# Performance work log

Hardware: AMD Instinct MI355X
Metric: run time of the kernel (lower is better)

Reference implementation:

```python
import jax, jax.numpy as jnp
import numpy as np

D_MODEL = 1024
N_HEADS = 16
HEAD = D_MODEL // N_HEADS
B, S = 2, 2048


def setup_inputs() -> dict:
    key = jax.random.key(0)
    ks = jax.random.split(key, 9)
    sc = 1.0 / np.sqrt(D_MODEL)
    return {
        "q": jax.random.normal(ks[0], (B, S, D_MODEL), dtype=jnp.float32),
        "k": jax.random.normal(ks[1], (B, S, D_MODEL), dtype=jnp.float32),
        "v": jax.random.normal(ks[2], (B, S, D_MODEL), dtype=jnp.float32),
        "mask": jnp.zeros((S, S), dtype=jnp.float32),
        "Wq": jax.random.normal(ks[3], (D_MODEL, D_MODEL), dtype=jnp.float32) * sc,
        "bq": jnp.zeros((D_MODEL,), dtype=jnp.float32),
        "Wk": jax.random.normal(ks[4], (D_MODEL, D_MODEL), dtype=jnp.float32) * sc,
        "bk": jnp.zeros((D_MODEL,), dtype=jnp.float32),
        "Wv": jax.random.normal(ks[5], (D_MODEL, D_MODEL), dtype=jnp.float32) * sc,
        "bv": jnpp_zeros() if False else jnp.zeros((D_MODEL,), dtype=jnp.float32),
    }


def reference(q, k, v, mask, Wq, bq, Wk, bk, Wv, bv):
    # Linear projections (torch Linear: x @ W.T + b)
    qp = q @ Wq.T + bq  # (B, S, D)
    kp = k @ Wk.T + bk
    vp = v @ Wv.T + bv
    # split heads -> (B, H, S, Hd)
    def split(x):
        return x.reshape(B, S, N_HEADS, HEAD).transpose(0, 2, 1, 3)
    qh, kh, vh = split(qp), split(kp), split(vp)
    scores = jnp.einsum('bhqd,bhkd->bhqk', qh, kh) / np.sqrt(HEAD)
    scores = scores + mask  # additive mask broadcast over (B, H)
    attn = jax.nn.softmax(scores, axis=-1)
    out = jnp.einsum('bhqk,bhkd->bhqd', attn, vh)
    return out.transpose(0, 2, 1, 3).reshape(B, S, D_MODEL)
```

## Files before the change

kernel.cpp:

```cpp
#include <hip/hip_runtime.h>
#include <cstdint>

#define DM 1024
#define NH 16
#define HDIM 64
#define SEQ 2048
#define NB 2
#define L2E 1.44269504f

typedef unsigned short u16;
typedef unsigned int u32;
typedef __attribute__((ext_vector_type(8))) short bf16x8;
typedef __attribute__((ext_vector_type(8))) unsigned short u16x8;
typedef __attribute__((ext_vector_type(4))) unsigned int u32x4;
typedef __attribute__((ext_vector_type(4))) float f32x4;
typedef __attribute__((ext_vector_type(16))) float f32x16;
typedef __attribute__((ext_vector_type(4))) unsigned short u16x4;

__device__ __forceinline__ u16 f2bf(float f) {
  uint32_t x = __float_as_uint(f);
  x += 0x7fffu + ((x >> 16) & 1u);
  return (u16)(x >> 16);
}

__device__ __forceinline__ u32 pack_bf2t(float lo, float hi) {
  return __builtin_amdgcn_perm(__float_as_uint(hi), __float_as_uint(lo), 0x07060302u);
}

__device__ __forceinline__ void gload_lds16(const void* g, void* lds) {
  __builtin_amdgcn_global_load_lds(
      (const __attribute__((address_space(1))) unsigned int*)(uintptr_t)g,
      (__attribute__((address_space(3))) unsigned int*)(uint32_t)(uintptr_t)lds,
      16, 0, 0);
}


__global__ __launch_bounds__(256) void cvt_kernel(
    const float4* __restrict__ s0, const float4* __restrict__ s1, const float4* __restrict__ s2,
    const float4* __restrict__ s3, const float4* __restrict__ s4, const float4* __restrict__ s5,
    u16x4* __restrict__ d0, u16x4* __restrict__ d1, u16x4* __restrict__ d2,
    u16x4* __restrict__ d3, u16x4* __restrict__ d4, u16x4* __restrict__ d5) {
  int i = blockIdx.x * 256 + threadIdx.x;
  const float4* s;
  u16x4* d;
  int off;
  if (i < 3 * 1048576) {
    int seg = i >> 20;
    off = i & 1048575;
    s = seg == 0 ? s0 : (seg == 1 ? s1 : s2);
    d = seg == 0 ? d0 : (seg == 1 ? d1 : d2);
  } else {
    int j = i - 3 * 1048576;
    int seg = j >> 18;
    off = j & 262143;
    s = seg == 0 ? s3 : (seg == 1 ? s4 : s5);
    d = seg == 0 ? d3 : (seg == 1 ? d4 : d5);
  }
  float4 v = s[off];
  u16x4 o = {f2bf(v.x), f2bf(v.y), f2bf(v.z), f2bf(v.w)};
  d[off] = o;
}

__global__ __launch_bounds__(256) void maskprep_kernel(const float* __restrict__ mask,
                                                       u16* __restrict__ maskP) {
  __shared__ float tile[32][257];
  const int t = threadIdx.x;
  const int q0 = blockIdx.x * 32;
#pragma unroll
  for (int ss = 0; ss < 2; ++ss) {
    const int st = blockIdx.y * 2 + ss;
    const int kv0 = st * 256;
    if (ss) __syncthreads();
#pragma unroll
    for (int p = 0; p < 8; ++p) {
      const int row = p * 4 + (t >> 6);
      const int col = (t & 63) * 4;
      *(float4*)&tile[row][col] = *(const float4*)&mask[(size_t)(q0 + row) * SEQ + kv0 + col];
    }
    __syncthreads();
    const int tgl = t >> 5, ql = t & 31;
    u16 outv[32];
#pragma unroll
    for (int i = 0; i < 32; ++i) {
      const int hl = i >> 4, r = i & 15;
      const int kvl = (r & 3) + 8 * (r >> 2) + 4 * hl;
      outv[i] = f2bf(tile[ql][tgl * 32 + kvl] * L2E);
    }
    u16* dst = maskP + ((size_t)(st * 8 + tgl) * SEQ + (q0 + ql)) * 32;
#pragma unroll
    for (int j = 0; j < 4; ++j) *(u16x8*)(dst + 8 * j) = *(const u16x8*)&outv[8 * j];
  }
}

__global__ __launch_bounds__(256) void proj_kernel(
    const u16* __restrict__ Xq, const u16* __restrict__ Xk, const u16* __restrict__ Xv,
    const u16* __restrict__ Wqp, const u16* __restrict__ Wkp, const u16* __restrict__ Wvp,
    const float* __restrict__ bqp, const float* __restrict__ bkp, const float* __restrict__ bvp,
    u16* __restrict__ Qp, u16* __restrict__ Kp, u16* __restrict__ Vt) {
  __shared__ __align__(16) u16 sA[2][128 * 32];
  __shared__ __align__(16) u16 sB[2][128 * 32];
  const int t = threadIdx.x;
  const int w = t >> 6, lane = t & 63, quad = lane >> 4, l16 = lane & 15;
  const int wr = w >> 1, wc = w & 1;
  const int m0 = blockIdx.y * 128, n0 = blockIdx.x * 128;
  const int mode = blockIdx.z;
  const u16* X = mode == 0 ? Xq : (mode == 1 ? Xk : Xv);
  const u16* W = mode == 0 ? Wqp : (mode == 1 ? Wkp : Wvp);
  const float* bias = mode == 0 ? bqp : (mode == 1 ? bkp : bvp);

  f32x4 acc[4][4] = {};
  const int srow = lane >> 2;
  const int scol = (lane & 3) * 16;

#pragma unroll
  for (int j = 0; j < 2; ++j) {
    const int rbase = (w * 2 + j) * 16;
    gload_lds16((const char*)X + ((size_t)(m0 + rbase + srow) * DM) * 2 + scol,
                (char*)sA[0] + rbase * 64);
    gload_lds16((const char*)W + ((size_t)(n0 + rbase + srow) * DM) * 2 + scol,
                (char*)sB[0] + rbase * 64);
  }

  for (int it = 0; it < 32; ++it) {
    const int p = it & 1;
    __syncthreads();
    if (it < 31) {
      const int k0 = (it + 1) * 32;
#pragma unroll
      for (int j = 0; j < 2; ++j) {
        const int rbase = (w * 2 + j) * 16;
        gload_lds16((const char*)X + ((size_t)(m0 + rbase + srow) * DM + k0) * 2 + scol,
                    (char*)sA[p ^ 1] + rbase * 64);
        gload_lds16((const char*)W + ((size_t)(n0 + rbase + srow) * DM + k0) * 2 + scol,
                    (char*)sB[p ^ 1] + rbase * 64);
      }
    }
    bf16x8 af[4], bfr[4];
#pragma unroll
    for (int i = 0; i < 4; ++i)
      af[i] = *(const bf16x8*)&sA[p][(wr * 64 + i * 16 + l16) * 32 + quad * 8];
#pragma unroll
    for (int j = 0; j < 4; ++j)
      bfr[j] = *(const bf16x8*)&sB[p][(wc * 64 + j * 16 + l16) * 32 + quad * 8];
#pragma unroll
    for (int i = 0; i < 4; ++i)
#pragma unroll
      for (int j = 0; j < 4; ++j)
        acc[i][j] = __builtin_amdgcn_mfma_f32_16x16x32_bf16(af[i], bfr[j], acc[i][j], 0, 0, 0);
  }

  float bb[4];
#pragma unroll
  for (int j = 0; j < 4; ++j) bb[j] = bias[n0 + wc * 64 + j * 16 + l16];
  const float scl = (mode == 0) ? 0.18033688011f : 1.0f;

#pragma unroll
  for (int i = 0; i < 4; ++i) {
    const int mbase = m0 + wr * 64 + i * 16 + quad * 4;
    const int bidx = mbase >> 11;
    const int s = mbase & 2047;
#pragma unroll
    for (int j = 0; j < 4; ++j) {
      const int n = n0 + wc * 64 + j * 16 + l16;
      const int h = n >> 6, hd = n & 63;
      const size_t hb = (size_t)(bidx * NH + h) * (SEQ * HDIM);
      if (mode == 2) {
        const int tv = (s >> 5) * 2048 + (hd >> 5) * 1024 + ((s >> 4) & 1) * 512 +
                       ((s >> 3) & 1) * 256 + (hd & 31) * 8 + (s & 7);
        u16x4 pk = {f2bf(acc[i][j][0] + bb[j]), f2bf(acc[i][j][1] + bb[j]),
                    f2bf(acc[i][j][2] + bb[j]), f2bf(acc[i][j][3] + bb[j])};
        *(u16x4*)&Vt[hb + tv] = pk;
      } else {
        u16* dst = (mode == 0) ? Qp : Kp;
        const int th = (s >> 5) * 2048 + (hd >> 4) * 512 + ((hd >> 3) & 1) * 256 +
                       (s & 31) * 8 + (hd & 7);
#pragma unroll
        for (int r = 0; r < 4; ++r)
          dst[hb + th + r * 8] = f2bf((acc[i][j][r] + bb[j]) * scl);
      }
    }
  }
}

__global__ __launch_bounds__(256, 2) void attn_kernel(
    const u16* __restrict__ Qp, const u16* __restrict__ Kp,
    const u16* __restrict__ Vt, const u16* __restrict__ maskP,
    float* __restrict__ out) {
  __shared__ float sO[4][32][65];
  __shared__ float sL[4][64];
  const int t = threadIdx.x, w = t >> 6, lane = t & 63;
  const int l31 = lane & 31, hl = lane >> 5;
  const int h = blockIdx.x, qt = blockIdx.y, b = blockIdx.z;
  const int q0 = qt * 64;
  const u16* Qh = Qp + (size_t)(b * NH + h) * (SEQ * HDIM);
  const u16* Kh = Kp + (size_t)(b * NH + h) * (SEQ * HDIM);
  const u16* Vh = Vt + (size_t)(b * NH + h) * (SEQ * HDIM);

  bf16x8 qf[2][4];
#pragma unroll
  for (int sub = 0; sub < 2; ++sub)
#pragma unroll
    for (int kt = 0; kt < 4; ++kt)
      qf[sub][kt] =
          *(const bf16x8*)(Qh + (size_t)((q0 >> 5) + sub) * 2048 + kt * 512 + lane * 8);

  const int Tb = w * 16;
  const u16* Kt = Kh + (size_t)Tb * 2048 + (size_t)lane * 8;
  const u16* Vw = Vh + (size_t)Tb * 2048 + (size_t)lane * 8;
  const u16* mb0 = maskP + ((size_t)Tb * SEQ + (q0 + l31)) * 32 + hl * 16;
  const u16* mb1 = mb0 + 32 * 32;

  f32x16 oacc[2][2] = {};
  float l_run[2] = {0.f, 0.f};

  bf16x8 kf[4], vf[2][2];
#pragma unroll
  for (int kt = 0; kt < 4; ++kt) kf[kt] = *(const bf16x8*)(Kt + kt * 512);
#pragma unroll
  for (int half = 0; half < 2; ++half)
#pragma unroll
    for (int ks = 0; ks < 2; ++ks)
      vf[half][ks] = *(const bf16x8*)(Vw + half * 1024 + ks * 512);
  u32x4 mk[2][2];
  mk[0][0] = *(const u32x4*)(mb0);
  mk[0][1] = *(const u32x4*)(mb0 + 8);
  mk[1][0] = *(const u32x4*)(mb1);
  mk[1][1] = *(const u32x4*)(mb1 + 8);

#pragma unroll 2
  for (int it = 0; it < 16; ++it) {
    const int itn = it < 15 ? it + 1 : 15;
    bf16x8 kfn[4], vfn[2][2];
#pragma unroll
    for (int kt = 0; kt < 4; ++kt)
      kfn[kt] = *(const bf16x8*)(Kt + (size_t)itn * 2048 + kt * 512);
#pragma unroll
    for (int half = 0; half < 2; ++half)
#pragma unroll
      for (int ks = 0; ks < 2; ++ks)
        vfn[half][ks] =
            *(const bf16x8*)(Vw + (size_t)itn * 2048 + half * 1024 + ks * 512);
    u32x4 mkn[2][2];
    mkn[0][0] = *(const u32x4*)(mb0 + (size_t)itn * (SEQ * 32));
    mkn[0][1] = *(const u32x4*)(mb0 + (size_t)itn * (SEQ * 32) + 8);
    mkn[1][0] = *(const u32x4*)(mb1 + (size_t)itn * (SEQ * 32));
    mkn[1][1] = *(const u32x4*)(mb1 + (size_t)itn * (SEQ * 32) + 8);

    bf16x8 pfr[2][2];
#pragma unroll
    for (int sub = 0; sub < 2; ++sub) {
      f32x16 st;
#pragma unroll
      for (int r = 0; r < 8; ++r) {
        const u32 word = (r < 4 ? mk[sub][0][r & 3] : mk[sub][1][r & 3]);
        st[2 * r] = __uint_as_float(word << 16);
        st[2 * r + 1] = __uint_as_float(word & 0xffff0000u);
      }
#pragma unroll
      for (int kt = 0; kt < 4; ++kt)
        st = __builtin_amdgcn_mfma_f32_32x32x16_bf16(kf[kt], qf[sub][kt], st, 0, 0, 0);

      float ls = 0.f;
#pragma unroll
      for (int r = 0; r < 16; ++r) {
        st[r] = __builtin_amdgcn_exp2f(st[r]);
        ls += st[r];
      }
      l_run[sub] += ls;

      u32 pk[4][2];
#pragma unroll
      for (int g = 0; g < 4; ++g) {
        pk[g][0] = pack_bf2t(st[4 * g + 0], st[4 * g + 1]);
        pk[g][1] = pack_bf2t(st[4 * g + 2], st[4 * g + 3]);
      }
#pragma unroll
      for (int ks = 0; ks < 2; ++ks) {
        u32 sa = hl ? pk[2 * ks][0] : pk[2 * ks + 1][0];
        u32 sb = hl ? pk[2 * ks][1] : pk[2 * ks + 1][1];
        u32 ra = __shfl_xor(sa, 32);
        u32 rb = __shfl_xor(sb, 32);
        u32 oa = hl ? pk[2 * ks + 1][0] : pk[2 * ks][0];
        u32 ob = hl ? pk[2 * ks + 1][1] : pk[2 * ks][1];
        union {
          u32 u[4];
          bf16x8 v;
        } f;
        f.u[0] = hl ? ra : oa;
        f.u[1] = hl ? rb : ob;
        f.u[2] = hl ? oa : ra;
        f.u[3] = hl ? ob : rb;
        pfr[sub][ks] = f.v;
      }
    }

#pragma unroll
    for (int sub = 0; sub < 2; ++sub)
#pragma unroll
      for (int ks = 0; ks < 2; ++ks) {
        oacc[0][sub] = __builtin_amdgcn_mfma_f32_32x32x16_bf16(vf[0][ks], pfr[sub][ks],
                                                               oacc[0][sub], 0, 0, 0);
        oacc[1][sub] = __builtin_amdgcn_mfma_f32_32x32x16_bf16(vf[1][ks], pfr[sub][ks],
                                                               oacc[1][sub], 0, 0, 0);
      }

#pragma unroll
    for (int kt = 0; kt < 4; ++kt) kf[kt] = kfn[kt];
#pragma unroll
    for (int half = 0; half < 2; ++half)
#pragma unroll
      for (int ks = 0; ks < 2; ++ks) vf[half][ks] = vfn[half][ks];
#pragma unroll
    for (int sub = 0; sub < 2; ++sub) {
      mk[sub][0] = mkn[sub][0];
      mk[sub][1] = mkn[sub][1];
    }
  }

  l_run[0] += __shfl_xor(l_run[0], 32);
  l_run[1] += __shfl_xor(l_run[1], 32);
  if (hl == 0) {
    sL[w][l31] = l_run[0];
    sL[w][32 + l31] = l_run[1];
  }

  const int hd = t & 31, grp = t >> 5;
#pragma unroll
  for (int half = 0; half < 2; ++half) {
    __syncthreads();
#pragma unroll
    for (int sub = 0; sub < 2; ++sub)
#pragma unroll
      for (int r = 0; r < 16; ++r)
        sO[w][(r & 3) + 8 * (r >> 2) + 4 * hl][sub * 32 + l31] = oacc[half][sub][r];
    __syncthreads();
#pragma unroll
    for (int p8 = 0; p8 < 8; ++p8) {
      const int qi = grp * 8 + p8;
      const float lsum = sL[0][qi] + sL[1][qi] + sL[2][qi] + sL[3][qi];
      const float val = sO[0][hd][qi] + sO[1][hd][qi] + sO[2][hd][qi] + sO[3][hd][qi];
      out[(size_t)(b * SEQ + q0 + qi) * DM + h * HDIM + half * 32 + hd] = val / lsum;
    }
  }
}

extern "C" void kernel_launch(void* const* d_in, const int* in_sizes, int n_in,
                              void* d_out, int out_size, void* d_ws, size_t ws_size,
                              hipStream_t stream) {
  const float* q = (const float*)d_in[0];
  const float* k = (const float*)d_in[1];
  const float* v = (const float*)d_in[2];
  const float* mask = (const float*)d_in[3];
  const float* Wq = (const float*)d_in[4];
  const float* bq = (const float*)d_in[5];
  const float* Wk = (const float*)d_in[6];
  const float* bk = (const float*)d_in[7];
  const float* Wv = (const float*)d_in[8];
  const float* bv = (const float*)d_in[9];

  char* ws = (char*)d_ws;
  u16* q_bf = (u16*)(ws + 0);
  u16* k_bf = (u16*)(ws + 8388608);
  u16* v_bf = (u16*)(ws + 16777216);
  u16* wq_bf = (u16*)(ws + 25165824);
  u16* wk_bf = (u16*)(ws + 27262976);
  u16* wv_bf = (u16*)(ws + 29360128);
  u16* Qp = (u16*)(ws + 31457280);
  u16* Kp = (u16*)(ws + 39845888);
  u16* Vt = (u16*)(ws + 48234496);
  u16* maskP = (u16*)(ws + 56623104);

  cvt_kernel<<<15360, 256, 0, stream>>>(
      (const float4*)q, (const float4*)k, (const float4*)v, (const float4*)Wq,
      (const float4*)Wk, (const float4*)Wv, (u16x4*)q_bf, (u16x4*)k_bf, (u16x4*)v_bf,
      (u16x4*)wq_bf, (u16x4*)wk_bf, (u16x4*)wv_bf);

  maskprep_kernel<<<dim3(64, 4), 256, 0, stream>>>(mask, maskP);

  proj_kernel<<<dim3(8, 32, 3), 256, 0, stream>>>(q_bf, k_bf, v_bf, wq_bf, wk_bf, wv_bf,
                                                  bq, bk, bv, Qp, Kp, Vt);

  attn_kernel<<<dim3(16, 32, 2), 256, 0, stream>>>(Qp, Kp, Vt, maskP, (float*)d_out);
}
```

Measured before the change: 217.5 us.

## Raise attention occupancy by dropping V prefetch and interleaving PV MFMAs

```diff
diff --git a/kernel.cpp b/kernel.cpp
--- a/kernel.cpp
+++ b/kernel.cpp
@@ -182,7 +182,7 @@
   }
 }
 
-__global__ __launch_bounds__(256, 2) void attn_kernel(
+__global__ __launch_bounds__(256, 3) void attn_kernel(
     const u16* __restrict__ Qp, const u16* __restrict__ Kp,
     const u16* __restrict__ Vt, const u16* __restrict__ maskP,
     float* __restrict__ out) {
@@ -205,48 +205,44 @@
           *(const bf16x8*)(Qh + (size_t)((q0 >> 5) + sub) * 2048 + kt * 512 + lane * 8);
 
   const int Tb = w * 16;
-  const u16* Kt = Kh + (size_t)Tb * 2048 + (size_t)lane * 8;
-  const u16* Vw = Vh + (size_t)Tb * 2048 + (size_t)lane * 8;
-  const u16* mb0 = maskP + ((size_t)Tb * SEQ + (q0 + l31)) * 32 + hl * 16;
-  const u16* mb1 = mb0 + 32 * 32;
+  const u16* Kc = Kh + (size_t)Tb * 2048 + (size_t)lane * 8;
+  const u16* Vc = Vh + (size_t)Tb * 2048 + (size_t)lane * 8;
+  const u16* m0c = maskP + ((size_t)Tb * SEQ + (q0 + l31)) * 32 + hl * 16;
+  const u16* m1c = m0c + 32 * 32;
 
   f32x16 oacc[2][2] = {};
   float l_run[2] = {0.f, 0.f};
 
-  bf16x8 kf[4], vf[2][2];
-#pragma unroll
-  for (int kt = 0; kt < 4; ++kt) kf[kt] = *(const bf16x8*)(Kt + kt * 512);
-#pragma unroll
-  for (int half = 0; half < 2; ++half)
-#pragma unroll
-    for (int ks = 0; ks < 2; ++ks)
-      vf[half][ks] = *(const bf16x8*)(Vw + half * 1024 + ks * 512);
+  bf16x8 kf[4];
+#pragma unroll
+  for (int kt = 0; kt < 4; ++kt) kf[kt] = *(const bf16x8*)(Kc + kt * 512);
   u32x4 mk[2][2];
-  mk[0][0] = *(const u32x4*)(mb0);
-  mk[0][1] = *(const u32x4*)(mb0 + 8);
-  mk[1][0] = *(const u32x4*)(mb1);
-  mk[1][1] = *(const u32x4*)(mb1 + 8);
+  mk[0][0] = *(const u32x4*)(m0c);
+  mk[0][1] = *(const u32x4*)(m0c + 8);
+  mk[1][0] = *(const u32x4*)(m1c);
+  mk[1][1] = *(const u32x4*)(m1c + 8);
 
 #pragma unroll 2
   for (int it = 0; it < 16; ++it) {
-    const int itn = it < 15 ? it + 1 : 15;
-    bf16x8 kfn[4], vfn[2][2];
-#pragma unroll
-    for (int kt = 0; kt < 4; ++kt)
-      kfn[kt] = *(const bf16x8*)(Kt + (size_t)itn * 2048 + kt * 512);
+    const int stepK = (it < 15) ? 2048 : 0;
+    const int stepM = (it < 15) ? (SEQ * 32) : 0;
+
+    bf16x8 vf[2][2];
 #pragma unroll
     for (int half = 0; half < 2; ++half)
 #pragma unroll
       for (int ks = 0; ks < 2; ++ks)
-        vfn[half][ks] =
-            *(const bf16x8*)(Vw + (size_t)itn * 2048 + half * 1024 + ks * 512);
+        vf[half][ks] = *(const bf16x8*)(Vc + half * 1024 + ks * 512);
+
+    bf16x8 kfn[4];
+#pragma unroll
+    for (int kt = 0; kt < 4; ++kt) kfn[kt] = *(const bf16x8*)(Kc + stepK + kt * 512);
     u32x4 mkn[2][2];
-    mkn[0][0] = *(const u32x4*)(mb0 + (size_t)itn * (SEQ * 32));
-    mkn[0][1] = *(const u32x4*)(mb0 + (size_t)itn * (SEQ * 32) + 8);
-    mkn[1][0] = *(const u32x4*)(mb1 + (size_t)itn * (SEQ * 32));
-    mkn[1][1] = *(const u32x4*)(mb1 + (size_t)itn * (SEQ * 32) + 8);
-
-    bf16x8 pfr[2][2];
+    mkn[0][0] = *(const u32x4*)(m0c + stepM);
+    mkn[0][1] = *(const u32x4*)(m0c + stepM + 8);
+    mkn[1][0] = *(const u32x4*)(m1c + stepM);
+    mkn[1][1] = *(const u32x4*)(m1c + stepM + 8);
+
 #pragma unroll
     for (int sub = 0; sub < 2; ++sub) {
       f32x16 st;
@@ -256,9 +252,11 @@
         st[2 * r] = __uint_as_float(word << 16);
         st[2 * r + 1] = __uint_as_float(word & 0xffff0000u);
       }
+      __builtin_amdgcn_s_setprio(1);
 #pragma unroll
       for (int kt = 0; kt < 4; ++kt)
         st = __builtin_amdgcn_mfma_f32_32x32x16_bf16(kf[kt], qf[sub][kt], st, 0, 0, 0);
+      __builtin_amdgcn_s_setprio(0);
 
       float ls = 0.f;
 #pragma unroll
@@ -290,31 +288,26 @@
         f.u[1] = hl ? rb : ob;
         f.u[2] = hl ? oa : ra;
         f.u[3] = hl ? ob : rb;
-        pfr[sub][ks] = f.v;
-      }
-    }
-
-#pragma unroll
-    for (int sub = 0; sub < 2; ++sub)
-#pragma unroll
-      for (int ks = 0; ks < 2; ++ks) {
-        oacc[0][sub] = __builtin_amdgcn_mfma_f32_32x32x16_bf16(vf[0][ks], pfr[sub][ks],
+        __builtin_amdgcn_s_setprio(1);
+        oacc[0][sub] = __builtin_amdgcn_mfma_f32_32x32x16_bf16(vf[0][ks], f.v,
                                                                oacc[0][sub], 0, 0, 0);
-        oacc[1][sub] = __builtin_amdgcn_mfma_f32_32x32x16_bf16(vf[1][ks], pfr[sub][ks],
+        oacc[1][sub] = __builtin_amdgcn_mfma_f32_32x32x16_bf16(vf[1][ks], f.v,
                                                                oacc[1][sub], 0, 0, 0);
-      }
+        __builtin_amdgcn_s_setprio(0);
+      }
+    }
 
 #pragma unroll
     for (int kt = 0; kt < 4; ++kt) kf[kt] = kfn[kt];
-#pragma unroll
-    for (int half = 0; half < 2; ++half)
-#pragma unroll
-      for (int ks = 0; ks < 2; ++ks) vf[half][ks] = vfn[half][ks];
 #pragma unroll
     for (int sub = 0; sub < 2; ++sub) {
       mk[sub][0] = mkn[sub][0];
       mk[sub][1] = mkn[sub][1];
     }
+    Kc += stepK;
+    Vc += 2048;
+    m0c += stepM;
+    m1c += stepM;
   }
 
   l_run[0] += __shfl_xor(l_run[0], 32);
```

New measurement: 464.1 us. +113.4%, slower.

## Remap projection block order and reload attention operands in place to cut registers

Applied to the files above, without the earlier changes.

```diff
diff --git a/kernel.cpp b/kernel.cpp
--- a/kernel.cpp
+++ b/kernel.cpp
@@ -102,8 +102,11 @@
   const int t = threadIdx.x;
   const int w = t >> 6, lane = t & 63, quad = lane >> 4, l16 = lane & 15;
   const int wr = w >> 1, wc = w & 1;
-  const int m0 = blockIdx.y * 128, n0 = blockIdx.x * 128;
-  const int mode = blockIdx.z;
+  const int hw = blockIdx.x + (blockIdx.y << 3) + (blockIdx.z << 8);
+  const int logical = (hw & 7) * 96 + (hw >> 3);
+  const int bx = logical & 7, by = (logical >> 3) & 31, bz = logical >> 8;
+  const int m0 = by * 128, n0 = bx * 128;
+  const int mode = bz;
   const u16* X = mode == 0 ? Xq : (mode == 1 ? Xk : Xv);
   const u16* W = mode == 0 ? Wqp : (mode == 1 ? Wkp : Wvp);
   const float* bias = mode == 0 ? bqp : (mode == 1 ? bkp : bvp);
@@ -230,21 +233,6 @@
 #pragma unroll 2
   for (int it = 0; it < 16; ++it) {
     const int itn = it < 15 ? it + 1 : 15;
-    bf16x8 kfn[4], vfn[2][2];
-#pragma unroll
-    for (int kt = 0; kt < 4; ++kt)
-      kfn[kt] = *(const bf16x8*)(Kt + (size_t)itn * 2048 + kt * 512);
-#pragma unroll
-    for (int half = 0; half < 2; ++half)
-#pragma unroll
-      for (int ks = 0; ks < 2; ++ks)
-        vfn[half][ks] =
-            *(const bf16x8*)(Vw + (size_t)itn * 2048 + half * 1024 + ks * 512);
-    u32x4 mkn[2][2];
-    mkn[0][0] = *(const u32x4*)(mb0 + (size_t)itn * (SEQ * 32));
-    mkn[0][1] = *(const u32x4*)(mb0 + (size_t)itn * (SEQ * 32) + 8);
-    mkn[1][0] = *(const u32x4*)(mb1 + (size_t)itn * (SEQ * 32));
-    mkn[1][1] = *(const u32x4*)(mb1 + (size_t)itn * (SEQ * 32) + 8);
 
     bf16x8 pfr[2][2];
 #pragma unroll
@@ -256,9 +244,19 @@
         st[2 * r] = __uint_as_float(word << 16);
         st[2 * r + 1] = __uint_as_float(word & 0xffff0000u);
       }
+      {
+        const u16* mb = (sub ? mb1 : mb0) + (size_t)itn * (SEQ * 32);
+        mk[sub][0] = *(const u32x4*)(mb);
+        mk[sub][1] = *(const u32x4*)(mb + 8);
+      }
 #pragma unroll
       for (int kt = 0; kt < 4; ++kt)
         st = __builtin_amdgcn_mfma_f32_32x32x16_bf16(kf[kt], qf[sub][kt], st, 0, 0, 0);
+      if (sub == 1) {
+#pragma unroll
+        for (int kt = 0; kt < 4; ++kt)
+          kf[kt] = *(const bf16x8*)(Kt + (size_t)itn * 2048 + kt * 512);
+      }
 
       float ls = 0.f;
 #pragma unroll
@@ -305,16 +303,11 @@
       }
 
 #pragma unroll
-    for (int kt = 0; kt < 4; ++kt) kf[kt] = kfn[kt];
-#pragma unroll
     for (int half = 0; half < 2; ++half)
 #pragma unroll
-      for (int ks = 0; ks < 2; ++ks) vf[half][ks] = vfn[half][ks];
-#pragma unroll
-    for (int sub = 0; sub < 2; ++sub) {
-      mk[sub][0] = mkn[sub][0];
-      mk[sub][1] = mkn[sub][1];
-    }
+      for (int ks = 0; ks < 2; ++ks)
+        vf[half][ks] =
+            *(const bf16x8*)(Vw + (size_t)itn * 2048 + half * 1024 + ks * 512);
   }
 
   l_run[0] += __shfl_xor(l_run[0], 32);
```

Result: no change. 219.8 us (+1.1%).
